# Performance work log

Measured on AMD Instinct MI355X. Metric: run time of the kernel, lower is better.

## Reference

```python
import jax, jax.numpy as jnp
import numpy as np

S = 8192        # seq_length
H2 = 1024       # 2 * lstm_hidden_size
A = 2048        # attention_hidden_size
E = 768         # embedding_dim == pos_embedding_dim


def _bahdanau_weights(sentence, length, ctx, W_s, b_s, W_c, b_c, v, b_v):
    # sentence: [1, S, H2], ctx: [1, E_ctx]
    u = jnp.einsum('bsh,ha->bsa', sentence, W_s) + b_s \
        + (ctx @ W_c + b_c)[:, None, :]                    # [1, S, A]
    e = jnp.einsum('bsa,a->bs', jnp.tanh(u), v) + b_v       # [1, S]
    mask = jnp.arange(S)[None, :] >= length[:, None]        # [1, S] key mask
    e = jnp.where(mask, -jnp.inf, e)
    all_inf = jnp.all(mask, axis=1)                         # [1]
    # guard fully-masked rows so softmax stays finite, then zero them (matches torch)
    e_safe = jnp.where(all_inf[:, None], jnp.zeros_like(e), e)
    w = jax.nn.softmax(e_safe, axis=1)
    return jnp.where(all_inf[:, None], 0.0, w)              # [1, S]


def setup_inputs() -> dict:
    key = jax.random.key(0)
    ks = jax.random.split(key, 24)
    f = jax.random.normal
    sc_s = 1.0 / np.sqrt(H2)
    sc_c = 1.0 / np.sqrt(E)
    sc_v = 1.0 / np.sqrt(A)
    inp = {
        'sentence': f(ks[0], (1, S, H2), jnp.float32),
        'length': jax.random.randint(ks[1], (1,), 0, S),
        'pos_embedding': f(ks[2], (1, E), jnp.float32),
        'cardinal_phrase_embedding': f(ks[3], (1, E), jnp.float32),
        'headline_embedding': f(ks[4], (1, E), jnp.float32),
    }
    i = 5
    for tag in ('p', 'c', 'h'):
        inp[f'W_sent_{tag}'] = f(ks[i], (H2, A), jnp.float32) * sc_s; i += 1
        inp[f'b_sent_{tag}'] = f(ks[i], (A,), jnp.float32) * sc_s; i += 1
        inp[f'W_ctx_{tag}'] = f(ks[i], (E, A), jnp.float32) * sc_c; i += 1
        inp[f'b_ctx_{tag}'] = f(ks[i], (A,), jnp.float32) * sc_c; i += 1
        inp[f'v_{tag}'] = f(ks[i], (A,), jnp.float32) * sc_v; i += 1
        inp[f'bv_{tag}'] = f(ks[i], (), jnp.float32) * sc_v; i += 1
    return inp


def reference(sentence, length, pos_embedding, cardinal_phrase_embedding,
              headline_embedding,
              W_sent_p, b_sent_p, W_ctx_p, b_ctx_p, v_p, bv_p,
              W_sent_c, b_sent_c, W_ctx_c, b_ctx_c, v_c, bv_c,
              W_sent_h, b_sent_h, W_ctx_h, b_ctx_h, v_h, bv_h):
    w_pos = _bahdanau_weights(sentence, length, pos_embedding,
                              W_sent_p, b_sent_p, W_ctx_p, b_ctx_p, v_p, bv_p)
    w_card = _bahdanau_weights(sentence, length, cardinal_phrase_embedding,
                               W_sent_c, b_sent_c, W_ctx_c, b_ctx_c, v_c, bv_c)
    w_head = _bahdanau_weights(sentence, length, headline_embedding,
                               W_sent_h, b_sent_h, W_ctx_h, b_ctx_h, v_h, bv_h)
    fused = (w_pos + w_card + w_head) / 3.0                 # [1, S]
    return jnp.einsum('bs,bsh->bh', fused, sentence)        # [1, H2]
```

## Files before the change

kernel.cpp:

```cpp
#include <hip/hip_runtime.h>
#include <hip/hip_bf16.h>
#include <stdint.h>


namespace {

constexpr int S = 8192;
constexpr int H = 1024;
constexpr int A = 2048;
constexpr int E = 768;

typedef __bf16 bf16x8 __attribute__((ext_vector_type(8)));
typedef float f32x4 __attribute__((ext_vector_type(4)));

__device__ __forceinline__ void gl_lds16(const void* g, void* l) {
  __builtin_amdgcn_global_load_lds(
      (const __attribute__((address_space(1))) void*)g,
      (__attribute__((address_space(3))) void*)l, 16, 0, 0);
}

__global__ __launch_bounds__(256)
void k_prep(const float* __restrict__ sentence, __bf16* __restrict__ sentB,
            const float* __restrict__ Wp, const float* __restrict__ Wc_s,
            const float* __restrict__ Wh, __bf16* __restrict__ WtB,
            const float* __restrict__ ctx_p, const float* __restrict__ ctx_c,
            const float* __restrict__ ctx_h,
            const float* __restrict__ Wcx_p, const float* __restrict__ Wcx_c,
            const float* __restrict__ Wcx_h,
            const float* __restrict__ bs_p, const float* __restrict__ bs_c,
            const float* __restrict__ bs_h,
            const float* __restrict__ bc_p, const float* __restrict__ bc_c,
            const float* __restrict__ bc_h,
            float* __restrict__ ctxb_q, float* __restrict__ e_arr,
            const int* __restrict__ length, float* __restrict__ out, int n_out) {
  __shared__ float tile[64][65];
  int b = blockIdx.x;
  int t = threadIdx.x;

  if (b < 4096) {
    int len = min(max(length[0], 0), S);
    int lenp = (len + 63) & ~63;
    if (b * 2 >= lenp) return;
    int g = b * 256 + t;
    const float4* s4 = (const float4*)sentence + (size_t)g * 2;
    float4 a = s4[0], c = s4[1];
    bf16x8 o;
    o[0] = (__bf16)a.x; o[1] = (__bf16)a.y; o[2] = (__bf16)a.z; o[3] = (__bf16)a.w;
    o[4] = (__bf16)c.x; o[5] = (__bf16)c.y; o[6] = (__bf16)c.z; o[7] = (__bf16)c.w;
    *((bf16x8*)sentB + g) = o;
  } else if (b < 5632) {
    int r = b - 4096;
    int head = r >> 9; r &= 511;
    const float* W = head == 0 ? Wp : (head == 1 ? Wc_s : Wh);
    __bf16* dst = WtB + (size_t)head * A * H;
    int a0 = (r & 31) * 64;
    int k0 = (r >> 5) * 64;
#pragma unroll
    for (int i = 0; i < 16; ++i) {
      int idx = t + i * 256;
      int rr = idx >> 6, cc = idx & 63;
      tile[cc][rr] = W[(size_t)(k0 + rr) * A + a0 + cc];
    }
    __syncthreads();
#pragma unroll
    for (int i = 0; i < 16; ++i) {
      int idx = t + i * 256;
      int al = idx >> 6, kl = idx & 63;
      dst[(size_t)(a0 + al) * H + k0 + kl] = (__bf16)tile[al][kl];
    }
  } else if (b < 5728) {
    int r = b - 5632;
    int head = r >> 5;
    int sub = r & 31;
    int ablk = sub & 7;
    int eq = sub >> 3;
    const float* ctx = head == 0 ? ctx_p : (head == 1 ? ctx_c : ctx_h);
    const float* Wc  = head == 0 ? Wcx_p : (head == 1 ? Wcx_c : Wcx_h);
    int a = ablk * 256 + t;
    float s = 0.f;
    if (eq == 0) {
      const float* bs = head == 0 ? bs_p : (head == 1 ? bs_c : bs_h);
      const float* bc = head == 0 ? bc_p : (head == 1 ? bc_c : bc_h);
      s = bs[a] + bc[a];
    }
    int e0 = eq * 192;
#pragma unroll 8
    for (int e = e0; e < e0 + 192; ++e) s = fmaf(ctx[e], Wc[(size_t)e * A + a], s);
    ctxb_q[eq * 3 * A + head * A + a] = s;
  } else {
    int idx = (b - 5728) * 256 + t;
    float4 z = {0.f, 0.f, 0.f, 0.f};
    int total = 6144 + (n_out >> 2);
    for (int i = idx; i < total; i += 2048) {
      if (i < 6144) ((float4*)e_arr)[i] = z;
      else ((float4*)out)[i - 6144] = z;
    }
  }
}

__global__ __launch_bounds__(256)
void k_gemm_e(const __bf16* __restrict__ sentB, const __bf16* __restrict__ WtB,
              const float* __restrict__ ctxb_q,
              const float* __restrict__ v_p, const float* __restrict__ v_c,
              const float* __restrict__ v_h,
              const int* __restrict__ length, float* __restrict__ e_out) {
  int m0 = blockIdx.x * 64;
  int len = min(max(length[0], 0), S);
  if (m0 >= len) return;
  int n0 = blockIdx.y * 64;
  int head = blockIdx.z;
  const float* v  = head == 0 ? v_p : (head == 1 ? v_c : v_h);
  const __bf16* Wt = WtB + (size_t)head * A * H;
  float* e_h = e_out + head * S;

  __shared__ __align__(16) __bf16 lsA[4 * 2048];
  __shared__ __align__(16) __bf16 lsB[4 * 2048];
  __shared__ float e_part[64];

  int tid = threadIdx.x;
  if (tid < 64) e_part[tid] = 0.f;

  int lane = tid & 63;
  int wave = tid >> 6;
  int wm = wave >> 1, wn = wave & 1;
  int quad = lane >> 4, l16 = lane & 15;

  f32x4 acc[2][2];
#pragma unroll
  for (int i = 0; i < 2; ++i)
#pragma unroll
    for (int j = 0; j < 2; ++j) acc[i][j] = (f32x4){0.f, 0.f, 0.f, 0.f};

  const __bf16* gA0 = sentB + (size_t)(m0 + (tid >> 2)) * H + ((tid & 3) * 8);
  const __bf16* gB0 = Wt + (size_t)(n0 + (tid >> 2)) * H + ((tid & 3) * 8);

#define STAGE(bufi, kk)                                           \
  do {                                                            \
    gl_lds16(gA0 + (kk), lsA + (bufi) * 2048 + tid * 8);          \
    gl_lds16(gB0 + (kk), lsB + (bufi) * 2048 + tid * 8);          \
  } while (0)

#define COMPUTE(bufi)                                                                          \
  do {                                                                                         \
    bf16x8 af[2], bfv[2];                                                                      \
    _Pragma("unroll")                                                                          \
    for (int i = 0; i < 2; ++i)                                                                \
      af[i] = *(const bf16x8*)&lsA[(bufi) * 2048 + (wm * 32 + i * 16 + l16) * 32 + quad * 8];  \
    _Pragma("unroll")                                                                          \
    for (int j = 0; j < 2; ++j)                                                                \
      bfv[j] = *(const bf16x8*)&lsB[(bufi) * 2048 + (wn * 32 + j * 16 + l16) * 32 + quad * 8]; \
    _Pragma("unroll")                                                                          \
    for (int i = 0; i < 2; ++i)                                                                \
      _Pragma("unroll")                                                                        \
      for (int j = 0; j < 2; ++j)                                                              \
        acc[i][j] = __builtin_amdgcn_mfma_f32_16x16x32_bf16(af[i], bfv[j], acc[i][j], 0, 0, 0);\
  } while (0)

  STAGE(0, 0);
  STAGE(1, 32);
  STAGE(2, 64);
#pragma unroll 1
  for (int t = 0; t < 29; ++t) {
    asm volatile("s_waitcnt vmcnt(4)");
    __builtin_amdgcn_s_barrier();
    __builtin_amdgcn_sched_barrier(0);
    STAGE((t + 3) & 3, (t + 3) * 32);
    COMPUTE(t & 3);
  }
  asm volatile("s_waitcnt vmcnt(4)");
  __builtin_amdgcn_s_barrier();
  __builtin_amdgcn_sched_barrier(0);
  COMPUTE(1);
  asm volatile("s_waitcnt vmcnt(2)");
  __builtin_amdgcn_s_barrier();
  __builtin_amdgcn_sched_barrier(0);
  COMPUTE(2);
  asm volatile("s_waitcnt vmcnt(0)");
  __builtin_amdgcn_s_barrier();
  __builtin_amdgcn_sched_barrier(0);
  COMPUTE(3);

#undef STAGE
#undef COMPUTE

  float vj[2], cbj[2];
#pragma unroll
  for (int j = 0; j < 2; ++j) {
    int col = n0 + wn * 32 + j * 16 + l16;
    vj[j] = v[col];
    cbj[j] = ctxb_q[head * A + col] + ctxb_q[3 * A + head * A + col] +
             ctxb_q[6 * A + head * A + col] + ctxb_q[9 * A + head * A + col];
  }
#pragma unroll
  for (int i = 0; i < 2; ++i) {
#pragma unroll
    for (int r = 0; r < 4; ++r) {
      float p = 0.f;
#pragma unroll
      for (int j = 0; j < 2; ++j) {
        float u = acc[i][j][r] + cbj[j];
        float ex = __expf(2.f * u);
        float th = 1.f - 2.f / (ex + 1.f);
        p = fmaf(th, vj[j], p);
      }
      p += __shfl_xor(p, 1);
      p += __shfl_xor(p, 2);
      p += __shfl_xor(p, 4);
      p += __shfl_xor(p, 8);
      if (l16 == 0) atomicAdd(&e_part[wm * 32 + i * 16 + quad * 4 + r], p);
    }
  }
  __syncthreads();
  if (tid < 64) atomicAdd(&e_h[m0 + tid], e_part[tid]);
}

__global__ void k_out(const float* __restrict__ sent, const float* __restrict__ e_arr,
                      const int* __restrict__ length, float* __restrict__ out) {
  int len = min(max(length[0], 0), S);
  int r0 = blockIdx.x * 16;
  if (r0 >= len) return;
  int tid = threadIdx.x;

  __shared__ float red[3][4];
  __shared__ float sstat[6];
  __shared__ float wrow[16];

#pragma unroll
  for (int h = 0; h < 3; ++h) {
    const float* e_h = e_arr + h * S;
    float m = -3.4e38f;
    for (int s = tid; s < len; s += 256) m = fmaxf(m, e_h[s]);
#pragma unroll
    for (int o = 32; o >= 1; o >>= 1) m = fmaxf(m, __shfl_xor(m, o));
    if ((tid & 63) == 0) red[h][tid >> 6] = m;
  }
  __syncthreads();
  if (tid < 3) sstat[tid * 2] = fmaxf(fmaxf(red[tid][0], red[tid][1]),
                                      fmaxf(red[tid][2], red[tid][3]));
  __syncthreads();
#pragma unroll
  for (int h = 0; h < 3; ++h) {
    const float* e_h = e_arr + h * S;
    float mm = sstat[h * 2];
    float ss = 0.f;
    for (int s = tid; s < len; s += 256) ss += __expf(e_h[s] - mm);
#pragma unroll
    for (int o = 32; o >= 1; o >>= 1) ss += __shfl_xor(ss, o);
    if ((tid & 63) == 0) red[h][tid >> 6] = ss;
  }
  __syncthreads();
  if (tid < 3) sstat[tid * 2 + 1] = red[tid][0] + red[tid][1] + red[tid][2] + red[tid][3];
  __syncthreads();

  if (tid < 16 && r0 + tid < len) {
    int r = r0 + tid;
    wrow[tid] = (__expf(e_arr[r] - sstat[0]) / sstat[1] +
                 __expf(e_arr[S + r] - sstat[2]) / sstat[3] +
                 __expf(e_arr[2 * S + r] - sstat[4]) / sstat[5]) * (1.f / 3.f);
  }
  __syncthreads();

  int col = tid * 4;
  int rend = min(r0 + 16, len);
  float4 acc = {0.f, 0.f, 0.f, 0.f};
  for (int r = r0; r < rend; ++r) {
    float w = wrow[r - r0];
    float4 x = *(const float4*)(sent + (size_t)r * H + col);
    acc.x = fmaf(w, x.x, acc.x);
    acc.y = fmaf(w, x.y, acc.y);
    acc.z = fmaf(w, x.z, acc.z);
    acc.w = fmaf(w, x.w, acc.w);
  }
  atomicAdd(&out[col + 0], acc.x);
  atomicAdd(&out[col + 1], acc.y);
  atomicAdd(&out[col + 2], acc.z);
  atomicAdd(&out[col + 3], acc.w);
}

}

extern "C" void kernel_launch(void* const* d_in, const int* in_sizes, int n_in,
                              void* d_out, int out_size, void* d_ws, size_t ws_size,
                              hipStream_t stream) {
  const float* sentence = (const float*)d_in[0];
  const int* length     = (const int*)d_in[1];
  const float* ctx_p = (const float*)d_in[2];
  const float* ctx_c = (const float*)d_in[3];
  const float* ctx_h = (const float*)d_in[4];
  const float* W_s[3] = {(const float*)d_in[5],  (const float*)d_in[11], (const float*)d_in[17]};
  const float* b_s[3] = {(const float*)d_in[6],  (const float*)d_in[12], (const float*)d_in[18]};
  const float* W_c[3] = {(const float*)d_in[7],  (const float*)d_in[13], (const float*)d_in[19]};
  const float* b_c[3] = {(const float*)d_in[8],  (const float*)d_in[14], (const float*)d_in[20]};
  const float* v_[3]  = {(const float*)d_in[9],  (const float*)d_in[15], (const float*)d_in[21]};
  float* out = (float*)d_out;

  char* ws = (char*)d_ws;
  __bf16* sentB  = (__bf16*)(ws);
  __bf16* WtB    = (__bf16*)(ws + 16777216);
  float* ctxb_q  = (float*)(ws + 29360128);
  float* e_arr   = (float*)(ws + 29458432);

  k_prep<<<5736, 256, 0, stream>>>(sentence, sentB,
                                   W_s[0], W_s[1], W_s[2], WtB,
                                   ctx_p, ctx_c, ctx_h,
                                   W_c[0], W_c[1], W_c[2],
                                   b_s[0], b_s[1], b_s[2],
                                   b_c[0], b_c[1], b_c[2], ctxb_q, e_arr,
                                   length, out, out_size);
  k_gemm_e<<<dim3(S / 64, A / 64, 3), 256, 0, stream>>>(sentB, WtB, ctxb_q,
                                                        v_[0], v_[1], v_[2], length, e_arr);
  k_out<<<S / 16, 256, 0, stream>>>(sentence, e_arr, length, out);
}
```

Measured before the change: 230.3 us.

## Pre-pack operands in MFMA fragment layout and load directly to registers

The prep kernel now writes the bf16 sentence and transposed weights in a layout where each 512-element segment already matches one 16x32 MFMA fragment, so the GEMM kernel loads operands straight from global memory into registers with no LDS staging and no barriers. The GEMM tile widens to 64x128 per block, with register double buffering, and block IDs are remapped so blocks sharing a weight panel sit on the same XCD for L2 reuse. The weight transpose also reads float2. This drops LDS traffic and synchronisation but relies on L2/global latency being hidden by the two-deep register prefetch, and it adds register pressure.

After: 213.7 us. 1.08x faster.

```diff
diff --git a/kernel.cpp b/kernel.cpp
--- a/kernel.cpp
+++ b/kernel.cpp
@@ -13,16 +13,17 @@
 typedef __bf16 bf16x8 __attribute__((ext_vector_type(8)));
 typedef float f32x4 __attribute__((ext_vector_type(4)));
 
-__device__ __forceinline__ void gl_lds16(const void* g, void* l) {
-  __builtin_amdgcn_global_load_lds(
-      (const __attribute__((address_space(1))) void*)g,
-      (__attribute__((address_space(3))) void*)l, 16, 0, 0);
+__device__ __forceinline__ bf16x8 cvt8(float4 lo, float4 hi) {
+  bf16x8 r;
+  r[0] = (__bf16)lo.x; r[1] = (__bf16)lo.y; r[2] = (__bf16)lo.z; r[3] = (__bf16)lo.w;
+  r[4] = (__bf16)hi.x; r[5] = (__bf16)hi.y; r[6] = (__bf16)hi.z; r[7] = (__bf16)hi.w;
+  return r;
 }
 
 __global__ __launch_bounds__(256)
-void k_prep(const float* __restrict__ sentence, __bf16* __restrict__ sentB,
+void k_prep(const float* __restrict__ sentence, __bf16* __restrict__ packA,
             const float* __restrict__ Wp, const float* __restrict__ Wc_s,
-            const float* __restrict__ Wh, __bf16* __restrict__ WtB,
+            const float* __restrict__ Wh, __bf16* __restrict__ packB,
             const float* __restrict__ ctx_p, const float* __restrict__ ctx_c,
             const float* __restrict__ ctx_h,
             const float* __restrict__ Wcx_p, const float* __restrict__ Wcx_c,
@@ -40,33 +41,43 @@
   if (b < 4096) {
     int len = min(max(length[0], 0), S);
     int lenp = (len + 63) & ~63;
-    if (b * 2 >= lenp) return;
-    int g = b * 256 + t;
-    const float4* s4 = (const float4*)sentence + (size_t)g * 2;
-    float4 a = s4[0], c = s4[1];
-    bf16x8 o;
-    o[0] = (__bf16)a.x; o[1] = (__bf16)a.y; o[2] = (__bf16)a.z; o[3] = (__bf16)a.w;
-    o[4] = (__bf16)c.x; o[5] = (__bf16)c.y; o[6] = (__bf16)c.z; o[7] = (__bf16)c.w;
-    *((bf16x8*)sentB + g) = o;
+    if ((b >> 4) * 32 >= lenp) return;
+    int C = b * 256 + t;
+    int seg = C >> 6;
+    int g = seg >> 6, kt = (seg >> 1) & 31, f = seg & 1;
+    int slot = C & 63, quad = slot >> 4, l16 = slot & 15;
+    const float4* s4 =
+        (const float4*)(sentence + (size_t)(g * 32 + f * 16 + l16) * H + kt * 32 + quad * 8);
+    *(bf16x8*)(packA + (size_t)seg * 512 + slot * 8) = cvt8(s4[0], s4[1]);
   } else if (b < 5632) {
     int r = b - 4096;
     int head = r >> 9; r &= 511;
     const float* W = head == 0 ? Wp : (head == 1 ? Wc_s : Wh);
-    __bf16* dst = WtB + (size_t)head * A * H;
     int a0 = (r & 31) * 64;
     int k0 = (r >> 5) * 64;
 #pragma unroll
-    for (int i = 0; i < 16; ++i) {
+    for (int i = 0; i < 8; ++i) {
       int idx = t + i * 256;
-      int rr = idx >> 6, cc = idx & 63;
-      tile[cc][rr] = W[(size_t)(k0 + rr) * A + a0 + cc];
+      int rr = idx >> 5;
+      int cc = (idx & 31) * 2;
+      float2 w2 = *(const float2*)&W[(size_t)(k0 + rr) * A + a0 + cc];
+      tile[cc][rr] = w2.x;
+      tile[cc + 1][rr] = w2.y;
     }
     __syncthreads();
 #pragma unroll
-    for (int i = 0; i < 16; ++i) {
-      int idx = t + i * 256;
-      int al = idx >> 6, kl = idx & 63;
-      dst[(size_t)(a0 + al) * H + k0 + kl] = (__bf16)tile[al][kl];
+    for (int i = 0; i < 2; ++i) {
+      int c = t + i * 256;
+      int segl = c >> 6;
+      int cgl = segl >> 1, ktl = segl & 1;
+      int slot = c & 63, quad = slot >> 4, l16 = slot & 15;
+      int al = cgl * 16 + l16;
+      int kl = ktl * 32 + quad * 8;
+      bf16x8 o;
+#pragma unroll
+      for (int e = 0; e < 8; ++e) o[e] = (__bf16)tile[al][kl + e];
+      size_t seg = ((size_t)head * 128 + (a0 >> 4) + cgl) * 32 + (k0 >> 5) + ktl;
+      *(bf16x8*)(packB + seg * 512 + slot * 8) = o;
     }
   } else if (b < 5728) {
     int r = b - 5632;
@@ -99,97 +110,103 @@
 }
 
 __global__ __launch_bounds__(256)
-void k_gemm_e(const __bf16* __restrict__ sentB, const __bf16* __restrict__ WtB,
+void k_gemm_e(const __bf16* __restrict__ packA, const __bf16* __restrict__ packB,
               const float* __restrict__ ctxb_q,
               const float* __restrict__ v_p, const float* __restrict__ v_c,
               const float* __restrict__ v_h,
               const int* __restrict__ length, float* __restrict__ e_out) {
-  int m0 = blockIdx.x * 64;
+  int bid = blockIdx.x;
+  int xcd = bid & 7;
+  int j = bid >> 3;
+  int mt = j / 6;
+  int pl = j - mt * 6;
+  int panel = xcd * 6 + pl;
+  int n0 = (panel & 15) * 128;
+  int head = panel >> 4;
+
+  int m0 = mt * 64;
   int len = min(max(length[0], 0), S);
   if (m0 >= len) return;
-  int n0 = blockIdx.y * 64;
-  int head = blockIdx.z;
   const float* v  = head == 0 ? v_p : (head == 1 ? v_c : v_h);
-  const __bf16* Wt = WtB + (size_t)head * A * H;
   float* e_h = e_out + head * S;
 
-  __shared__ __align__(16) __bf16 lsA[4 * 2048];
-  __shared__ __align__(16) __bf16 lsB[4 * 2048];
   __shared__ float e_part[64];
 
   int tid = threadIdx.x;
   if (tid < 64) e_part[tid] = 0.f;
+  __syncthreads();
 
   int lane = tid & 63;
   int wave = tid >> 6;
   int wm = wave >> 1, wn = wave & 1;
   int quad = lane >> 4, l16 = lane & 15;
 
-  f32x4 acc[2][2];
+  f32x4 acc[2][4];
 #pragma unroll
   for (int i = 0; i < 2; ++i)
 #pragma unroll
-    for (int j = 0; j < 2; ++j) acc[i][j] = (f32x4){0.f, 0.f, 0.f, 0.f};
-
-  const __bf16* gA0 = sentB + (size_t)(m0 + (tid >> 2)) * H + ((tid & 3) * 8);
-  const __bf16* gB0 = Wt + (size_t)(n0 + (tid >> 2)) * H + ((tid & 3) * 8);
-
-#define STAGE(bufi, kk)                                           \
-  do {                                                            \
-    gl_lds16(gA0 + (kk), lsA + (bufi) * 2048 + tid * 8);          \
-    gl_lds16(gB0 + (kk), lsB + (bufi) * 2048 + tid * 8);          \
+    for (int j2 = 0; j2 < 4; ++j2) acc[i][j2] = (f32x4){0.f, 0.f, 0.f, 0.f};
+
+  const __bf16* gA = packA + ((size_t)(m0 >> 5) + wm) * 64 * 512 + (size_t)lane * 8;
+  const __bf16* gB =
+      packB + (((size_t)head * 128 + (n0 >> 4) + wn * 4) * 32) * 512 + (size_t)lane * 8;
+
+  bf16x8 xa0, xa1, ya0, ya1;
+  bf16x8 xb0, xb1, xb2, xb3, yb0, yb1, yb2, yb3;
+
+#define LOADA(sl, kt)                                   \
+  do {                                                  \
+    sl##0 = *(const bf16x8*)(gA + ((kt) << 10));        \
+    sl##1 = *(const bf16x8*)(gA + ((kt) << 10) + 512);  \
   } while (0)
 
-#define COMPUTE(bufi)                                                                          \
-  do {                                                                                         \
-    bf16x8 af[2], bfv[2];                                                                      \
-    _Pragma("unroll")                                                                          \
-    for (int i = 0; i < 2; ++i)                                                                \
-      af[i] = *(const bf16x8*)&lsA[(bufi) * 2048 + (wm * 32 + i * 16 + l16) * 32 + quad * 8];  \
-    _Pragma("unroll")                                                                          \
-    for (int j = 0; j < 2; ++j)                                                                \
-      bfv[j] = *(const bf16x8*)&lsB[(bufi) * 2048 + (wn * 32 + j * 16 + l16) * 32 + quad * 8]; \
-    _Pragma("unroll")                                                                          \
-    for (int i = 0; i < 2; ++i)                                                                \
-      _Pragma("unroll")                                                                        \
-      for (int j = 0; j < 2; ++j)                                                              \
-        acc[i][j] = __builtin_amdgcn_mfma_f32_16x16x32_bf16(af[i], bfv[j], acc[i][j], 0, 0, 0);\
+#define LOADB(sl, kt)                                        \
+  do {                                                       \
+    sl##0 = *(const bf16x8*)(gB + ((size_t)(kt) << 9));          \
+    sl##1 = *(const bf16x8*)(gB + ((size_t)(32 + (kt)) << 9));   \
+    sl##2 = *(const bf16x8*)(gB + ((size_t)(64 + (kt)) << 9));   \
+    sl##3 = *(const bf16x8*)(gB + ((size_t)(96 + (kt)) << 9));   \
   } while (0)
 
-  STAGE(0, 0);
-  STAGE(1, 32);
-  STAGE(2, 64);
+#define COMPUTE(asl, bsl)                                                                     \
+  do {                                                                                        \
+    acc[0][0] = __builtin_amdgcn_mfma_f32_16x16x32_bf16(asl##0, bsl##0, acc[0][0], 0, 0, 0);  \
+    acc[1][0] = __builtin_amdgcn_mfma_f32_16x16x32_bf16(asl##1, bsl##0, acc[1][0], 0, 0, 0);  \
+    acc[0][1] = __builtin_amdgcn_mfma_f32_16x16x32_bf16(asl##0, bsl##1, acc[0][1], 0, 0, 0);  \
+    acc[1][1] = __builtin_amdgcn_mfma_f32_16x16x32_bf16(asl##1, bsl##1, acc[1][1], 0, 0, 0);  \
+    acc[0][2] = __builtin_amdgcn_mfma_f32_16x16x32_bf16(asl##0, bsl##2, acc[0][2], 0, 0, 0);  \
+    acc[1][2] = __builtin_amdgcn_mfma_f32_16x16x32_bf16(asl##1, bsl##2, acc[1][2], 0, 0, 0);  \
+    acc[0][3] = __builtin_amdgcn_mfma_f32_16x16x32_bf16(asl##0, bsl##3, acc[0][3], 0, 0, 0);  \
+    acc[1][3] = __builtin_amdgcn_mfma_f32_16x16x32_bf16(asl##1, bsl##3, acc[1][3], 0, 0, 0);  \
+  } while (0)
+
+  LOADA(xa, 0);
+  LOADB(xb, 0);
 #pragma unroll 1
-  for (int t = 0; t < 29; ++t) {
-    asm volatile("s_waitcnt vmcnt(4)");
-    __builtin_amdgcn_s_barrier();
-    __builtin_amdgcn_sched_barrier(0);
-    STAGE((t + 3) & 3, (t + 3) * 32);
-    COMPUTE(t & 3);
-  }
-  asm volatile("s_waitcnt vmcnt(4)");
-  __builtin_amdgcn_s_barrier();
-  __builtin_amdgcn_sched_barrier(0);
-  COMPUTE(1);
-  asm volatile("s_waitcnt vmcnt(2)");
-  __builtin_amdgcn_s_barrier();
-  __builtin_amdgcn_sched_barrier(0);
-  COMPUTE(2);
-  asm volatile("s_waitcnt vmcnt(0)");
-  __builtin_amdgcn_s_barrier();
-  __builtin_amdgcn_sched_barrier(0);
-  COMPUTE(3);
-
-#undef STAGE
+  for (int kt = 0; kt < 30; kt += 2) {
+    LOADA(ya, kt + 1);
+    LOADB(yb, kt + 1);
+    COMPUTE(xa, xb);
+    LOADA(xa, kt + 2);
+    LOADB(xb, kt + 2);
+    COMPUTE(ya, yb);
+  }
+  LOADA(ya, 31);
+  LOADB(yb, 31);
+  COMPUTE(xa, xb);
+  COMPUTE(ya, yb);
+
+#undef LOADA
+#undef LOADB
 #undef COMPUTE
 
-  float vj[2], cbj[2];
-#pragma unroll
-  for (int j = 0; j < 2; ++j) {
-    int col = n0 + wn * 32 + j * 16 + l16;
-    vj[j] = v[col];
-    cbj[j] = ctxb_q[head * A + col] + ctxb_q[3 * A + head * A + col] +
-             ctxb_q[6 * A + head * A + col] + ctxb_q[9 * A + head * A + col];
+  float vj[4], cbj[4];
+#pragma unroll
+  for (int j2 = 0; j2 < 4; ++j2) {
+    int col = n0 + wn * 64 + j2 * 16 + l16;
+    vj[j2] = v[col];
+    cbj[j2] = ctxb_q[head * A + col] + ctxb_q[3 * A + head * A + col] +
+              ctxb_q[6 * A + head * A + col] + ctxb_q[9 * A + head * A + col];
   }
 #pragma unroll
   for (int i = 0; i < 2; ++i) {
@@ -197,11 +214,11 @@
     for (int r = 0; r < 4; ++r) {
       float p = 0.f;
 #pragma unroll
-      for (int j = 0; j < 2; ++j) {
-        float u = acc[i][j][r] + cbj[j];
+      for (int j2 = 0; j2 < 4; ++j2) {
+        float u = acc[i][j2][r] + cbj[j2];
         float ex = __expf(2.f * u);
         float th = 1.f - 2.f / (ex + 1.f);
-        p = fmaf(th, vj[j], p);
+        p = fmaf(th, vj[j2], p);
       }
       p += __shfl_xor(p, 1);
       p += __shfl_xor(p, 2);
@@ -295,19 +312,19 @@
   float* out = (float*)d_out;
 
   char* ws = (char*)d_ws;
-  __bf16* sentB  = (__bf16*)(ws);
-  __bf16* WtB    = (__bf16*)(ws + 16777216);
+  __bf16* packA  = (__bf16*)(ws);
+  __bf16* packB  = (__bf16*)(ws + 16777216);
   float* ctxb_q  = (float*)(ws + 29360128);
   float* e_arr   = (float*)(ws + 29458432);
 
-  k_prep<<<5736, 256, 0, stream>>>(sentence, sentB,
-                                   W_s[0], W_s[1], W_s[2], WtB,
+  k_prep<<<5736, 256, 0, stream>>>(sentence, packA,
+                                   W_s[0], W_s[1], W_s[2], packB,
                                    ctx_p, ctx_c, ctx_h,
                                    W_c[0], W_c[1], W_c[2],
                                    b_s[0], b_s[1], b_s[2],
                                    b_c[0], b_c[1], b_c[2], ctxb_q, e_arr,
                                    length, out, out_size);
-  k_gemm_e<<<dim3(S / 64, A / 64, 3), 256, 0, stream>>>(sentB, WtB, ctxb_q,
-                                                        v_[0], v_[1], v_[2], length, e_arr);
+  k_gemm_e<<<6144, 256, 0, stream>>>(packA, packB, ctxb_q,
+                                     v_[0], v_[1], v_[2], length, e_arr);
   k_out<<<S / 16, 256, 0, stream>>>(sentence, e_arr, length, out);
 }
```
